# Performance work log

Measured on AMD Instinct MI355X. Metric: run time of the kernel, lower is better.

Reference implementation:

```python
import jax, jax.numpy as jnp
import numpy as np

B, S, E = 2, 2048, 2048
H, D = 16, 128  # num_heads, head_dim = E // H


def setup_inputs() -> dict:
    key = jax.random.key(0)
    ks = jax.random.split(key, 5)
    hidden_states = jax.random.normal(ks[0], (B, S, E), dtype=jnp.float32) * 0.02
    wq = jax.random.normal(ks[1], (E, E), dtype=jnp.float32) * 0.02
    wk = jax.random.normal(ks[2], (E, E), dtype=jnp.float32) * 0.02
    wv = jax.random.normal(ks[3], (E, E), dtype=jnp.float32) * 0.02
    wo = jax.random.normal(ks[4], (E, E), dtype=jnp.float32) * 0.02
    bo = jnp.zeros((E,), dtype=jnp.float32)
    return {"hidden_states": hidden_states, "wq": wq, "wk": wk, "wv": wv, "wo": wo, "bo": bo}


def _split_heads(x):
    # [B, S, E] -> [B, H, S, D]
    return x.reshape(B, S, H, D).transpose(0, 2, 1, 3)


def reference(hidden_states, wq, wk, wv, wo, bo):
    q = _split_heads(hidden_states @ wq)  # [B,H,S,D]
    k = _split_heads(hidden_states @ wk)
    v = _split_heads(hidden_states @ wv)

    # GPT-Neo: no 1/sqrt(d) scaling; scores computed in fp32
    attn_weights = jnp.einsum("bhqd,bhkd->bhqk", q.astype(jnp.float32), k.astype(jnp.float32))

    causal_mask = jnp.tril(jnp.ones((S, S), dtype=bool))  # bias[:, :, :S, :S]
    # Faithful quirk: masked positions get the GLOBAL MIN of attn_weights, not -inf
    mask_value = jnp.min(attn_weights)
    attn_weights = jnp.where(causal_mask, attn_weights, mask_value)

    attn_weights = jax.nn.softmax(attn_weights, axis=-1).astype(v.dtype)
    attn_output = jnp.einsum("bhqk,bhkd->bhqd", attn_weights, v)  # [B,H,S,D]

    # merge heads: [B,H,S,D] -> [B,S,E]
    attn_output = attn_output.transpose(0, 2, 1, 3).reshape(B, S, E)
    attn_output = attn_output @ wo + bo
    return attn_output
```

## Files before the change

kernel.cpp:

```cpp
#include <hip/hip_runtime.h>

typedef unsigned short u16;
typedef unsigned int   u32;
typedef __attribute__((ext_vector_type(4))) float f32x4;
typedef __attribute__((ext_vector_type(4))) u32   u32x4;
typedef __attribute__((ext_vector_type(8))) __bf16 bf16x8;

#define S_LEN 2048
#define EMB   2048
#define NH    16
#define HD    128
#define NBH   32
#define MTOT  4096

__device__ __forceinline__ u16 f2bf(float f) {
    u32 u = __float_as_uint(f);
    return (u16)((u + 0x7FFFu + ((u >> 16) & 1u)) >> 16);
}
__device__ __forceinline__ float bf2f(u16 v) {
    return __uint_as_float(((u32)v) << 16);
}
__device__ __forceinline__ bf16x8 ld_frag(const u16* p) {
    return __builtin_bit_cast(bf16x8, *(const u32x4*)p);
}
__device__ __forceinline__ void gld_lds16(const void* g, void* l) {
    __builtin_amdgcn_global_load_lds(
        (__attribute__((address_space(1))) void*)(g),
        (__attribute__((address_space(3))) void*)(l), 16, 0, 0);
}

__global__ __launch_bounds__(256) void cast_x_kernel(
    const float* __restrict__ X, u16* __restrict__ Xb)
{
    const size_t i = ((size_t)blockIdx.x * 256 + threadIdx.x) * 8;
    float4 a = *(const float4*)&X[i];
    float4 b = *(const float4*)&X[i + 4];
    u32x4 o;
    o.x = (u32)f2bf(a.x) | ((u32)f2bf(a.y) << 16);
    o.y = (u32)f2bf(a.z) | ((u32)f2bf(a.w) << 16);
    o.z = (u32)f2bf(b.x) | ((u32)f2bf(b.y) << 16);
    o.w = (u32)f2bf(b.z) | ((u32)f2bf(b.w) << 16);
    *(u32x4*)&Xb[i] = o;
}

__global__ __launch_bounds__(256) void transpose_cast_w_kernel(
    const float* __restrict__ W0, const float* __restrict__ W1,
    const float* __restrict__ W2, const float* __restrict__ W3,
    u16* __restrict__ T0, u16* __restrict__ T1,
    u16* __restrict__ T2, u16* __restrict__ T3)
{
    __shared__ float Ls[64][68];
    const int t = threadIdx.x;
    const int n0 = blockIdx.x * 64, k0 = blockIdx.y * 64;
    const int z = blockIdx.z;
    const float* __restrict__ W = (z == 0) ? W0 : (z == 1) ? W1 : (z == 2) ? W2 : W3;
    u16* __restrict__ T = (z == 0) ? T0 : (z == 1) ? T1 : (z == 2) ? T2 : T3;

#pragma unroll
    for (int p = 0; p < 4; ++p) {
        const int r = (t >> 4) + 16 * p;
        const int c = (t & 15) * 4;
        *(float4*)&Ls[r][c] = *(const float4*)&W[(size_t)(k0 + r) * EMB + n0 + c];
    }
    __syncthreads();
    const int nl = t >> 2, q = t & 3;
    u32 pk[8];
#pragma unroll
    for (int j = 0; j < 8; ++j) {
        u16 lo = f2bf(Ls[q * 16 + 2 * j][nl]);
        u16 hi = f2bf(Ls[q * 16 + 2 * j + 1][nl]);
        pk[j] = (u32)lo | ((u32)hi << 16);
    }
    u32x4 o0 = {pk[0], pk[1], pk[2], pk[3]};
    u32x4 o1 = {pk[4], pk[5], pk[6], pk[7]};
    u16* dst = &T[(size_t)(n0 + nl) * EMB + k0 + q * 16];
    *(u32x4*)&dst[0] = o0;
    *(u32x4*)&dst[8] = o1;
}

__global__ __launch_bounds__(256) void transpose_v_kernel(
    const u16* __restrict__ V, u16* __restrict__ Vt)
{
    __shared__ u16 Ls[64][72];
    const int t = threadIdx.x;
    const int s0 = blockIdx.x * 64, d0 = blockIdx.y * 64, bh = blockIdx.z;
    const u16* __restrict__ src0 = V + ((size_t)bh * S_LEN) * HD;
    {
        const int r = t >> 2, c0 = (t & 3) * 16;
        const u16* src = &src0[(size_t)(s0 + r) * HD + d0 + c0];
        *(u32x4*)&Ls[r][c0]     = *(const u32x4*)&src[0];
        *(u32x4*)&Ls[r][c0 + 8] = *(const u32x4*)&src[8];
    }
    __syncthreads();
    const int dl = t >> 2, q = t & 3;
    u32 pk[8];
#pragma unroll
    for (int j = 0; j < 8; ++j) {
        u16 lo = Ls[q * 16 + 2 * j][dl];
        u16 hi = Ls[q * 16 + 2 * j + 1][dl];
        pk[j] = (u32)lo | ((u32)hi << 16);
    }
    u32x4 o0 = {pk[0], pk[1], pk[2], pk[3]};
    u32x4 o1 = {pk[4], pk[5], pk[6], pk[7]};
    u16* dst = &Vt[((size_t)bh * HD + d0 + dl) * S_LEN + s0 + q * 16];
    *(u32x4*)&dst[0] = o0;
    *(u32x4*)&dst[8] = o1;
}

__global__ __launch_bounds__(256) void gemm_qkv_mfma(
    const u16* __restrict__ Xb,
    const u16* __restrict__ Wtq, const u16* __restrict__ Wtk,
    const u16* __restrict__ Wtv,
    u16* __restrict__ Qo, u16* __restrict__ Ko, u16* __restrict__ Vo)
{
    __shared__ __attribute__((aligned(16))) u16 As[128 * 32];
    __shared__ __attribute__((aligned(16))) u16 Bs[128 * 32];
    const int t = threadIdx.x;
    const int w = t >> 6, lane = t & 63;
    const int wy = w >> 1, wx = w & 1;
    const int n0 = blockIdx.x * 128, m0 = blockIdx.y * 128;
    const int z = blockIdx.z;
    const u16* __restrict__ Wt = (z == 0) ? Wtq : (z == 1) ? Wtk : Wtv;
    u16* __restrict__ O = (z == 0) ? Qo : (z == 1) ? Ko : Vo;

    const int srow = lane >> 2, scol = (lane & 3) * 8;
    const u16* Ag = &Xb[(size_t)(m0 + w * 32 + srow) * EMB + scol];
    const u16* Bg = &Wt[(size_t)(n0 + w * 32 + srow) * EMB + scol];
    u16* Al0 = &As[(w * 32) * 32];
    u16* Al1 = &As[(w * 32 + 16) * 32];
    u16* Bl0 = &Bs[(w * 32) * 32];
    u16* Bl1 = &Bs[(w * 32 + 16) * 32];

    const int fm = lane & 15, fk = (lane >> 4) * 8;
    f32x4 acc[4][4];
#pragma unroll
    for (int i = 0; i < 4; ++i)
#pragma unroll
        for (int j = 0; j < 4; ++j) acc[i][j] = (f32x4)0.0f;

    for (int k0 = 0; k0 < EMB; k0 += 32) {
        __syncthreads();
        gld_lds16(Ag + k0, Al0);
        gld_lds16(Ag + 16 * EMB + k0, Al1);
        gld_lds16(Bg + k0, Bl0);
        gld_lds16(Bg + 16 * EMB + k0, Bl1);
        __syncthreads();
        bf16x8 af[4], bfr[4];
#pragma unroll
        for (int mi = 0; mi < 4; ++mi)
            af[mi] = ld_frag(&As[(64 * wy + 16 * mi + fm) * 32 + fk]);
#pragma unroll
        for (int ni = 0; ni < 4; ++ni)
            bfr[ni] = ld_frag(&Bs[(64 * wx + 16 * ni + fm) * 32 + fk]);
#pragma unroll
        for (int mi = 0; mi < 4; ++mi)
#pragma unroll
            for (int ni = 0; ni < 4; ++ni)
                acc[mi][ni] = __builtin_amdgcn_mfma_f32_16x16x32_bf16(
                    af[mi], bfr[ni], acc[mi][ni], 0, 0, 0);
    }

    const int q4 = (lane >> 4) * 4;
#pragma unroll
    for (int mi = 0; mi < 4; ++mi)
#pragma unroll
        for (int ni = 0; ni < 4; ++ni) {
            const int n = n0 + 64 * wx + 16 * ni + (lane & 15);
            const int h = n >> 7, d = n & 127;
#pragma unroll
            for (int r = 0; r < 4; ++r) {
                const int m = m0 + 64 * wy + 16 * mi + q4 + r;
                const int bb = m >> 11, s = m & 2047;
                O[(((size_t)(bb * NH + h) * S_LEN) + s) * HD + d] = f2bf(acc[mi][ni][r]);
            }
        }
}

__global__ __launch_bounds__(256) void gemm_out_mfma(
    const u16* __restrict__ Ab, const u16* __restrict__ Wto,
    const float* __restrict__ bias, float* __restrict__ Out)
{
    __shared__ __attribute__((aligned(16))) u16 As[128 * 32];
    __shared__ __attribute__((aligned(16))) u16 Bs[128 * 32];
    const int t = threadIdx.x;
    const int w = t >> 6, lane = t & 63;
    const int wy = w >> 1, wx = w & 1;
    const int n0 = blockIdx.x * 128, m0 = blockIdx.y * 128;

    const int srow = lane >> 2, scol = (lane & 3) * 8;
    const u16* Ag = &Ab[(size_t)(m0 + w * 32 + srow) * EMB + scol];
    const u16* Bg = &Wto[(size_t)(n0 + w * 32 + srow) * EMB + scol];
    u16* Al0 = &As[(w * 32) * 32];
    u16* Al1 = &As[(w * 32 + 16) * 32];
    u16* Bl0 = &Bs[(w * 32) * 32];
    u16* Bl1 = &Bs[(w * 32 + 16) * 32];

    const int fm = lane & 15, fk = (lane >> 4) * 8;
    f32x4 acc[4][4];
#pragma unroll
    for (int i = 0; i < 4; ++i)
#pragma unroll
        for (int j = 0; j < 4; ++j) acc[i][j] = (f32x4)0.0f;

    for (int k0 = 0; k0 < EMB; k0 += 32) {
        __syncthreads();
        gld_lds16(Ag + k0, Al0);
        gld_lds16(Ag + 16 * EMB + k0, Al1);
        gld_lds16(Bg + k0, Bl0);
        gld_lds16(Bg + 16 * EMB + k0, Bl1);
        __syncthreads();
        bf16x8 af[4], bfr[4];
#pragma unroll
        for (int mi = 0; mi < 4; ++mi)
            af[mi] = ld_frag(&As[(64 * wy + 16 * mi + fm) * 32 + fk]);
#pragma unroll
        for (int ni = 0; ni < 4; ++ni)
            bfr[ni] = ld_frag(&Bs[(64 * wx + 16 * ni + fm) * 32 + fk]);
#pragma unroll
        for (int mi = 0; mi < 4; ++mi)
#pragma unroll
            for (int ni = 0; ni < 4; ++ni)
                acc[mi][ni] = __builtin_amdgcn_mfma_f32_16x16x32_bf16(
                    af[mi], bfr[ni], acc[mi][ni], 0, 0, 0);
    }

    const int q4 = (lane >> 4) * 4;
#pragma unroll
    for (int mi = 0; mi < 4; ++mi)
#pragma unroll
        for (int ni = 0; ni < 4; ++ni) {
            const int n = n0 + 64 * wx + 16 * ni + (lane & 15);
            const float bv = bias[n];
#pragma unroll
            for (int r = 0; r < 4; ++r) {
                const int m = m0 + 64 * wy + 16 * mi + q4 + r;
                Out[(size_t)m * EMB + n] = acc[mi][ni][r] + bv;
            }
        }
}

__global__ __launch_bounds__(256) void qk_min_mfma(
    const u16* __restrict__ Q, const u16* __restrict__ K,
    float* __restrict__ blockmin)
{
    __shared__ __attribute__((aligned(16))) u16 As[128 * 32];
    __shared__ __attribute__((aligned(16))) u16 Bs[128 * 32];
    __shared__ float sm[256];
    const int t = threadIdx.x;
    const int w = t >> 6, lane = t & 63;
    const int wy = w >> 1, wx = w & 1;
    const int kt = blockIdx.x, qt = blockIdx.y, bh = blockIdx.z;

    const int srow = lane >> 2, scol = (lane & 3) * 8;
    const u16* Ag = &Q[((size_t)bh * S_LEN + qt * 128 + w * 32 + srow) * HD + scol];
    const u16* Bg = &K[((size_t)bh * S_LEN + kt * 128 + w * 32 + srow) * HD + scol];
    u16* Al0 = &As[(w * 32) * 32];
    u16* Al1 = &As[(w * 32 + 16) * 32];
    u16* Bl0 = &Bs[(w * 32) * 32];
    u16* Bl1 = &Bs[(w * 32 + 16) * 32];

    const int fm = lane & 15, fk = (lane >> 4) * 8;
    f32x4 acc[4][4];
#pragma unroll
    for (int i = 0; i < 4; ++i)
#pragma unroll
        for (int j = 0; j < 4; ++j) acc[i][j] = (f32x4)0.0f;

    for (int k0 = 0; k0 < HD; k0 += 32) {
        __syncthreads();
        gld_lds16(Ag + k0, Al0);
        gld_lds16(Ag + 16 * HD + k0, Al1);
        gld_lds16(Bg + k0, Bl0);
        gld_lds16(Bg + 16 * HD + k0, Bl1);
        __syncthreads();
        bf16x8 af[4], bfr[4];
#pragma unroll
        for (int mi = 0; mi < 4; ++mi)
            af[mi] = ld_frag(&As[(64 * wy + 16 * mi + fm) * 32 + fk]);
#pragma unroll
        for (int ni = 0; ni < 4; ++ni)
            bfr[ni] = ld_frag(&Bs[(64 * wx + 16 * ni + fm) * 32 + fk]);
#pragma unroll
        for (int mi = 0; mi < 4; ++mi)
#pragma unroll
            for (int ni = 0; ni < 4; ++ni)
                acc[mi][ni] = __builtin_amdgcn_mfma_f32_16x16x32_bf16(
                    af[mi], bfr[ni], acc[mi][ni], 0, 0, 0);
    }

    float mn = acc[0][0][0];
#pragma unroll
    for (int mi = 0; mi < 4; ++mi)
#pragma unroll
        for (int ni = 0; ni < 4; ++ni)
#pragma unroll
            for (int r = 0; r < 4; ++r) mn = fminf(mn, acc[mi][ni][r]);
    sm[t] = mn;
    __syncthreads();
    for (int sft = 128; sft > 0; sft >>= 1) {
        if (t < sft) sm[t] = fminf(sm[t], sm[t + sft]);
        __syncthreads();
    }
    if (t == 0) blockmin[((size_t)bh * 16 + qt) * 16 + kt] = sm[0];
}

__global__ __launch_bounds__(256) void reduce_min_kernel(
    const float* __restrict__ bm, float* __restrict__ minval)
{
    __shared__ float sm[256];
    const int t = threadIdx.x;
    float m = 3.0e38f;
    for (int i = t; i < 16 * 16 * NBH; i += 256) m = fminf(m, bm[i]);
    sm[t] = m;
    __syncthreads();
    for (int sft = 128; sft > 0; sft >>= 1) {
        if (t < sft) sm[t] = fminf(sm[t], sm[t + sft]);
        __syncthreads();
    }
    if (t == 0) minval[0] = sm[0];
}

__global__ __launch_bounds__(128) void vchunk_sum_kernel(
    const u16* __restrict__ V, float* __restrict__ csum)
{
    const int chunk = blockIdx.x, bh = blockIdx.y, d = threadIdx.x;
    const u16* vb = V + ((size_t)bh * S_LEN + chunk * 64) * HD + d;
    float s = 0.0f;
    for (int r = 0; r < 64; ++r) s += bf2f(vb[(size_t)r * HD]);
    csum[((size_t)bh * 32 + chunk) * HD + d] = s;
}

__global__ __launch_bounds__(128) void vchunk_suffix_kernel(
    const float* __restrict__ csum, float* __restrict__ csuf)
{
    const int bh = blockIdx.x, d = threadIdx.x;
    float run = 0.0f;
    for (int c = 31; c >= 0; --c) {
        const size_t idx = ((size_t)bh * 32 + c) * HD + d;
        csuf[idx] = run;
        run += csum[idx];
    }
}

__global__ __launch_bounds__(128) void vsuffix_kernel(
    const u16* __restrict__ V, const float* __restrict__ csuf,
    float* __restrict__ vsuf)
{
    const int chunk = blockIdx.x, bh = blockIdx.y, d = threadIdx.x;
    float run = csuf[((size_t)bh * 32 + chunk) * HD + d];
    const size_t base = ((size_t)bh * S_LEN + chunk * 64) * HD + d;
    for (int r = 63; r >= 0; --r) {
        vsuf[base + (size_t)r * HD] = run;
        run += bf2f(V[base + (size_t)r * HD]);
    }
}

__global__ __launch_bounds__(256) void attn_mfma(
    const u16* __restrict__ Q, const u16* __restrict__ K,
    const u16* __restrict__ Vt, const float* __restrict__ vsuf,
    const float* __restrict__ minval, u16* __restrict__ outm)
{
    __shared__ __attribute__((aligned(16))) u16 Qs[128 * 136];
    __shared__ __attribute__((aligned(16))) u16 Ps[128 * 136];
    __shared__ __attribute__((aligned(16))) u16 Cs[128 * 32];
    __shared__ float den_l[2][128];

    const int t = threadIdx.x;
    const int w = t >> 6, lane = t & 63;
    const int wy = w >> 1, wx = w & 1;
    const int qt = blockIdx.x, bh = blockIdx.y;
    const int b = bh >> 4, h = bh & 15;
    const int i0 = qt * 128;

    const u16* __restrict__ Qg  = Q + ((size_t)bh * S_LEN + i0) * HD;
    const u16* __restrict__ Kg  = K + (size_t)bh * S_LEN * HD;
    const u16* __restrict__ Vtg = Vt + (size_t)bh * HD * S_LEN;

    {
        const int r = t >> 1, ch = (t & 1) * 64;
        const u16* src = &Qg[(size_t)r * HD + ch];
        u16* dst = &Qs[r * 136 + ch];
#pragma unroll
        for (int j = 0; j < 8; ++j)
            *(u32x4*)&dst[j * 8] = *(const u32x4*)&src[j * 8];
    }

    const int srow = lane >> 2, scol = (lane & 3) * 8;
    const int fm = lane & 15, fk = (lane >> 4) * 8;
    const int q4 = (lane >> 4) * 4;

    f32x4 oacc[4][4];
#pragma unroll
    for (int i = 0; i < 4; ++i)
#pragma unroll
        for (int j = 0; j < 4; ++j) oacc[i][j] = (f32x4)0.0f;
    float den[4][4] = {};

    const int ntile = qt + 1;
    for (int jt = 0; jt < ntile; ++jt) {
        const int j0 = jt * 128;
        f32x4 sacc[4][4];
#pragma unroll
        for (int i = 0; i < 4; ++i)
#pragma unroll
            for (int j = 0; j < 4; ++j) sacc[i][j] = (f32x4)0.0f;
        for (int dk = 0; dk < 4; ++dk) {
            __syncthreads();
            {
                const u16* g = &Kg[(size_t)(j0 + w * 32 + srow) * HD + dk * 32 + scol];
                gld_lds16(g, &Cs[(w * 32) * 32]);
                gld_lds16(g + 16 * HD, &Cs[(w * 32 + 16) * 32]);
            }
            __syncthreads();
            bf16x8 af[4], bfr[4];
#pragma unroll
            for (int mi = 0; mi < 4; ++mi)
                af[mi] = ld_frag(&Qs[(64 * wy + 16 * mi + fm) * 136 + dk * 32 + fk]);
#pragma unroll
            for (int ni = 0; ni < 4; ++ni)
                bfr[ni] = ld_frag(&Cs[(64 * wx + 16 * ni + fm) * 32 + fk]);
#pragma unroll
            for (int mi = 0; mi < 4; ++mi)
#pragma unroll
                for (int ni = 0; ni < 4; ++ni)
                    sacc[mi][ni] = __builtin_amdgcn_mfma_f32_16x16x32_bf16(
                        af[mi], bfr[ni], sacc[mi][ni], 0, 0, 0);
        }
        const bool dg = (jt == qt);
#pragma unroll
        for (int mi = 0; mi < 4; ++mi) {
            const int rbase = 64 * wy + 16 * mi + q4;
#pragma unroll
            for (int ni = 0; ni < 4; ++ni) {
                const int cl = 64 * wx + 16 * ni + (lane & 15);
                const int jg = j0 + cl;
#pragma unroll
                for (int r = 0; r < 4; ++r) {
                    float e = __expf(sacc[mi][ni][r]);
                    if (dg && jg > i0 + rbase + r) e = 0.0f;
                    den[mi][r] += e;
                    Ps[(rbase + r) * 136 + cl] = f2bf(e);
                }
            }
        }
        for (int sk = 0; sk < 4; ++sk) {
            __syncthreads();
            {
                const u16* g = &Vtg[(size_t)(w * 32 + srow) * S_LEN + j0 + sk * 32 + scol];
                gld_lds16(g, &Cs[(w * 32) * 32]);
                gld_lds16(g + 16 * S_LEN, &Cs[(w * 32 + 16) * 32]);
            }
            __syncthreads();
            bf16x8 pa[4], pb[4];
#pragma unroll
            for (int mi = 0; mi < 4; ++mi)
                pa[mi] = ld_frag(&Ps[(64 * wy + 16 * mi + fm) * 136 + sk * 32 + fk]);
#pragma unroll
            for (int ni = 0; ni < 4; ++ni)
                pb[ni] = ld_frag(&Cs[(64 * wx + 16 * ni + fm) * 32 + fk]);
#pragma unroll
            for (int mi = 0; mi < 4; ++mi)
#pragma unroll
                for (int ni = 0; ni < 4; ++ni)
                    oacc[mi][ni] = __builtin_amdgcn_mfma_f32_16x16x32_bf16(
                        pa[mi], pb[ni], oacc[mi][ni], 0, 0, 0);
        }
    }

#pragma unroll
    for (int mi = 0; mi < 4; ++mi)
#pragma unroll
        for (int r = 0; r < 4; ++r) {
            float v = den[mi][r];
            v += __shfl_xor(v, 1, 64);
            v += __shfl_xor(v, 2, 64);
            v += __shfl_xor(v, 4, 64);
            v += __shfl_xor(v, 8, 64);
            den[mi][r] = v;
        }
    __syncthreads();
    if ((lane & 15) == 0) {
#pragma unroll
        for (int mi = 0; mi < 4; ++mi)
#pragma unroll
            for (int r = 0; r < 4; ++r)
                den_l[wx][64 * wy + 16 * mi + q4 + r] = den[mi][r];
    }
    __syncthreads();

    const float em = __expf(minval[0]);
#pragma unroll
    for (int mi = 0; mi < 4; ++mi)
#pragma unroll
        for (int ni = 0; ni < 4; ++ni) {
            const int d = 64 * wx + 16 * ni + (lane & 15);
#pragma unroll
            for (int r = 0; r < 4; ++r) {
                const int row = 64 * wy + 16 * mi + q4 + r;
                const int ig = i0 + row;
                const float dt = den_l[0][row] + den_l[1][row]
                               + (float)(S_LEN - 1 - ig) * em;
                const float sv = vsuf[((size_t)bh * S_LEN + ig) * HD + d];
                const float o = (oacc[mi][ni][r] + em * sv) / dt;
                outm[((size_t)b * S_LEN + ig) * EMB + h * HD + d] = f2bf(o);
            }
        }
}

extern "C" void kernel_launch(void* const* d_in, const int* in_sizes, int n_in,
                              void* d_out, int out_size, void* d_ws, size_t ws_size,
                              hipStream_t stream)
{
    (void)in_sizes; (void)n_in; (void)out_size; (void)ws_size;
    const float* hs = (const float*)d_in[0];
    const float* wq = (const float*)d_in[1];
    const float* wk = (const float*)d_in[2];
    const float* wv = (const float*)d_in[3];
    const float* wo = (const float*)d_in[4];
    const float* bo = (const float*)d_in[5];
    float* out = (float*)d_out;

    char* p = (char*)d_ws;
    const size_t TS = (size_t)NBH * S_LEN * HD;
    u16* Xb   = (u16*)p; p += (size_t)MTOT * EMB * 2;
    u16* Wtq  = (u16*)p; p += (size_t)EMB * EMB * 2;
    u16* Wtk  = (u16*)p; p += (size_t)EMB * EMB * 2;
    u16* Wtv  = (u16*)p; p += (size_t)EMB * EMB * 2;
    u16* Wto  = (u16*)p; p += (size_t)EMB * EMB * 2;
    u16* Qb   = (u16*)p; p += TS * 2;
    u16* Kb   = (u16*)p; p += TS * 2;
    u16* Vb   = (u16*)p; p += TS * 2;
    u16* Vtb  = (u16*)p; p += TS * 2;
    u16* outm = (u16*)p; p += (size_t)MTOT * EMB * 2;
    float* vsuf     = (float*)p; p += TS * 4;
    float* csum     = (float*)p; p += (size_t)NBH * 32 * HD * 4;
    float* csuf     = (float*)p; p += (size_t)NBH * 32 * HD * 4;
    float* blockmin = (float*)p; p += 8192 * 4;
    float* minval   = (float*)p; p += 64;

    cast_x_kernel<<<4096, 256, 0, stream>>>(hs, Xb);
    transpose_cast_w_kernel<<<dim3(32, 32, 4), 256, 0, stream>>>(
        wq, wk, wv, wo, Wtq, Wtk, Wtv, Wto);

    gemm_qkv_mfma<<<dim3(EMB / 128, MTOT / 128, 3), 256, 0, stream>>>(
        Xb, Wtq, Wtk, Wtv, Qb, Kb, Vb);

    transpose_v_kernel<<<dim3(32, 2, NBH), 256, 0, stream>>>(Vb, Vtb);
    vchunk_sum_kernel<<<dim3(32, NBH), 128, 0, stream>>>(Vb, csum);
    vchunk_suffix_kernel<<<NBH, 128, 0, stream>>>(csum, csuf);
    vsuffix_kernel<<<dim3(32, NBH), 128, 0, stream>>>(Vb, csuf, vsuf);

    qk_min_mfma<<<dim3(16, 16, NBH), 256, 0, stream>>>(Qb, Kb, blockmin);
    reduce_min_kernel<<<1, 256, 0, stream>>>(blockmin, minval);

    attn_mfma<<<dim3(S_LEN / 128, NBH), 256, 0, stream>>>(
        Qb, Kb, Vtb, vsuf, minval, outm);

    gemm_out_mfma<<<dim3(EMB / 128, MTOT / 128), 256, 0, stream>>>(
        outm, Wto, bo, out);
}
```

Baseline: 482.6 us.

## Fuse lower-triangle min into attention and balance causal tiles with split-K passes

The global-min pass now only computes QK scores for strictly upper-triangular tiles. The attention kernel computes the lower-triangle minimum as it goes, which removes the duplicated score work. The attention grid pairs query tile pp with tile 15-pp to balance causal work across blocks. Each pair is split by key-tile parity into two partial accumulators, stored in bf16 together with partial denominators. A new finalize kernel then combines the partials with the suffix-V correction and the global min. This adds extra memory traffic and an extra bf16 rounding of the partial outputs.

```diff
diff --git a/kernel.cpp b/kernel.cpp
--- a/kernel.cpp
+++ b/kernel.cpp
@@ -12,6 +12,8 @@
 #define HD    128
 #define NBH   32
 #define MTOT  4096
+#define NUP   120
+#define NBMIN (NBH * NUP + 512)
 
 __device__ __forceinline__ u16 f2bf(float f) {
     u32 u = __float_as_uint(f);
@@ -239,7 +241,7 @@
         }
 }
 
-__global__ __launch_bounds__(256) void qk_min_mfma(
+__global__ __launch_bounds__(256) void qk_upper_min(
     const u16* __restrict__ Q, const u16* __restrict__ K,
     float* __restrict__ blockmin)
 {
@@ -249,7 +251,10 @@
     const int t = threadIdx.x;
     const int w = t >> 6, lane = t & 63;
     const int wy = w >> 1, wx = w & 1;
-    const int kt = blockIdx.x, qt = blockIdx.y, bh = blockIdx.z;
+    int u = blockIdx.x, qt = 0, cnt = 15;
+    while (u >= cnt) { u -= cnt; ++qt; cnt = 15 - qt; }
+    const int kt = qt + 1 + u;
+    const int bh = blockIdx.y;
 
     const int srow = lane >> 2, scol = (lane & 3) * 8;
     const u16* Ag = &Q[((size_t)bh * S_LEN + qt * 128 + w * 32 + srow) * HD + scol];
@@ -301,7 +306,7 @@
         if (t < sft) sm[t] = fminf(sm[t], sm[t + sft]);
         __syncthreads();
     }
-    if (t == 0) blockmin[((size_t)bh * 16 + qt) * 16 + kt] = sm[0];
+    if (t == 0) blockmin[(size_t)bh * NUP + blockIdx.x] = sm[0];
 }
 
 __global__ __launch_bounds__(256) void reduce_min_kernel(
@@ -310,7 +315,7 @@
     __shared__ float sm[256];
     const int t = threadIdx.x;
     float m = 3.0e38f;
-    for (int i = t; i < 16 * 16 * NBH; i += 256) m = fminf(m, bm[i]);
+    for (int i = t; i < NBMIN; i += 256) m = fminf(m, bm[i]);
     sm[t] = m;
     __syncthreads();
     for (int sft = 128; sft > 0; sft >>= 1) {
@@ -357,154 +362,205 @@
 
 __global__ __launch_bounds__(256) void attn_mfma(
     const u16* __restrict__ Q, const u16* __restrict__ K,
-    const u16* __restrict__ Vt, const float* __restrict__ vsuf,
-    const float* __restrict__ minval, u16* __restrict__ outm)
+    const u16* __restrict__ Vt,
+    u16* __restrict__ pacc0, u16* __restrict__ pacc1,
+    float* __restrict__ den_p, float* __restrict__ blockmin)
 {
     __shared__ __attribute__((aligned(16))) u16 Qs[128 * 136];
     __shared__ __attribute__((aligned(16))) u16 Ps[128 * 136];
     __shared__ __attribute__((aligned(16))) u16 Cs[128 * 32];
     __shared__ float den_l[2][128];
+    __shared__ float smn[256];
 
     const int t = threadIdx.x;
     const int w = t >> 6, lane = t & 63;
     const int wy = w >> 1, wx = w & 1;
-    const int qt = blockIdx.x, bh = blockIdx.y;
+    const int pp = blockIdx.x >> 1, hpar = blockIdx.x & 1;
+    const int bh = blockIdx.y;
     const int b = bh >> 4, h = bh & 15;
-    const int i0 = qt * 128;
-
-    const u16* __restrict__ Qg  = Q + ((size_t)bh * S_LEN + i0) * HD;
+
     const u16* __restrict__ Kg  = K + (size_t)bh * S_LEN * HD;
     const u16* __restrict__ Vtg = Vt + (size_t)bh * HD * S_LEN;
-
-    {
-        const int r = t >> 1, ch = (t & 1) * 64;
-        const u16* src = &Qg[(size_t)r * HD + ch];
-        u16* dst = &Qs[r * 136 + ch];
-#pragma unroll
-        for (int j = 0; j < 8; ++j)
-            *(u32x4*)&dst[j * 8] = *(const u32x4*)&src[j * 8];
-    }
+    u16* __restrict__ pacc = hpar ? pacc1 : pacc0;
 
     const int srow = lane >> 2, scol = (lane & 3) * 8;
     const int fm = lane & 15, fk = (lane >> 4) * 8;
     const int q4 = (lane >> 4) * 4;
 
-    f32x4 oacc[4][4];
-#pragma unroll
-    for (int i = 0; i < 4; ++i)
-#pragma unroll
-        for (int j = 0; j < 4; ++j) oacc[i][j] = (f32x4)0.0f;
-    float den[4][4] = {};
-
-    const int ntile = qt + 1;
-    for (int jt = 0; jt < ntile; ++jt) {
-        const int j0 = jt * 128;
-        f32x4 sacc[4][4];
+    float mn = 3.0e38f;
+
+    for (int pass = 0; pass < 2; ++pass) {
+        const int qt = pass ? (15 - pp) : pp;
+        const int i0 = qt * 128;
+        const u16* __restrict__ Qg = Q + ((size_t)bh * S_LEN + i0) * HD;
+
+        __syncthreads();
+        {
+            const int r = t >> 1, ch = (t & 1) * 64;
+            const u16* src = &Qg[(size_t)r * HD + ch];
+            u16* dst = &Qs[r * 136 + ch];
+#pragma unroll
+            for (int j = 0; j < 8; ++j)
+                *(u32x4*)&dst[j * 8] = *(const u32x4*)&src[j * 8];
+        }
+
+        f32x4 oacc[4][4];
 #pragma unroll
         for (int i = 0; i < 4; ++i)
 #pragma unroll
-            for (int j = 0; j < 4; ++j) sacc[i][j] = (f32x4)0.0f;
-        for (int dk = 0; dk < 4; ++dk) {
-            __syncthreads();
-            {
-                const u16* g = &Kg[(size_t)(j0 + w * 32 + srow) * HD + dk * 32 + scol];
-                gld_lds16(g, &Cs[(w * 32) * 32]);
-                gld_lds16(g + 16 * HD, &Cs[(w * 32 + 16) * 32]);
+            for (int j = 0; j < 4; ++j) oacc[i][j] = (f32x4)0.0f;
+        float den[4][4] = {};
+
+        for (int jt = hpar; jt <= qt; jt += 2) {
+            const int j0 = jt * 128;
+            f32x4 sacc[4][4];
+#pragma unroll
+            for (int i = 0; i < 4; ++i)
+#pragma unroll
+                for (int j = 0; j < 4; ++j) sacc[i][j] = (f32x4)0.0f;
+            for (int dk = 0; dk < 4; ++dk) {
+                __syncthreads();
+                {
+                    const u16* g = &Kg[(size_t)(j0 + w * 32 + srow) * HD + dk * 32 + scol];
+                    gld_lds16(g, &Cs[(w * 32) * 32]);
+                    gld_lds16(g + 16 * HD, &Cs[(w * 32 + 16) * 32]);
+                }
+                __syncthreads();
+                bf16x8 af[4], bfr[4];
+#pragma unroll
+                for (int mi = 0; mi < 4; ++mi)
+                    af[mi] = ld_frag(&Qs[(64 * wy + 16 * mi + fm) * 136 + dk * 32 + fk]);
+#pragma unroll
+                for (int ni = 0; ni < 4; ++ni)
+                    bfr[ni] = ld_frag(&Cs[(64 * wx + 16 * ni + fm) * 32 + fk]);
+#pragma unroll
+                for (int mi = 0; mi < 4; ++mi)
+#pragma unroll
+                    for (int ni = 0; ni < 4; ++ni)
+                        sacc[mi][ni] = __builtin_amdgcn_mfma_f32_16x16x32_bf16(
+                            af[mi], bfr[ni], sacc[mi][ni], 0, 0, 0);
+            }
+            const bool dg = (jt == qt);
+#pragma unroll
+            for (int mi = 0; mi < 4; ++mi) {
+                const int rbase = 64 * wy + 16 * mi + q4;
+#pragma unroll
+                for (int ni = 0; ni < 4; ++ni) {
+                    const int cl = 64 * wx + 16 * ni + (lane & 15);
+                    const int jg = j0 + cl;
+#pragma unroll
+                    for (int r = 0; r < 4; ++r) {
+                        const float s = sacc[mi][ni][r];
+                        mn = fminf(mn, s);
+                        float e = __expf(s);
+                        if (dg && jg > i0 + rbase + r) e = 0.0f;
+                        den[mi][r] += e;
+                        Ps[(rbase + r) * 136 + cl] = f2bf(e);
+                    }
+                }
             }
             __syncthreads();
-            bf16x8 af[4], bfr[4];
+
+            for (int sk = 0; sk < 4; ++sk) {
+                if (sk) __syncthreads();
+                {
+                    const u16* g = &Vtg[(size_t)(w * 32 + srow) * S_LEN + j0 + sk * 32 + scol];
+                    gld_lds16(g, &Cs[(w * 32) * 32]);
+                    gld_lds16(g + 16 * S_LEN, &Cs[(w * 32 + 16) * 32]);
+                }
+                __syncthreads();
+                bf16x8 pa[4], pb[4];
+#pragma unroll
+                for (int mi = 0; mi < 4; ++mi)
+                    pa[mi] = ld_frag(&Ps[(64 * wy + 16 * mi + fm) * 136 + sk * 32 + fk]);
+#pragma unroll
+                for (int ni = 0; ni < 4; ++ni)
+                    pb[ni] = ld_frag(&Cs[(64 * wx + 16 * ni + fm) * 32 + fk]);
+#pragma unroll
+                for (int mi = 0; mi < 4; ++mi)
+#pragma unroll
+                    for (int ni = 0; ni < 4; ++ni)
+                        oacc[mi][ni] = __builtin_amdgcn_mfma_f32_16x16x32_bf16(
+                            pa[mi], pb[ni], oacc[mi][ni], 0, 0, 0);
+            }
+        }
+
+#pragma unroll
+        for (int mi = 0; mi < 4; ++mi)
+#pragma unroll
+            for (int r = 0; r < 4; ++r) {
+                float v = den[mi][r];
+                v += __shfl_xor(v, 1, 64);
+                v += __shfl_xor(v, 2, 64);
+                v += __shfl_xor(v, 4, 64);
+                v += __shfl_xor(v, 8, 64);
+                den[mi][r] = v;
+            }
+        __syncthreads();
+        if ((lane & 15) == 0) {
 #pragma unroll
             for (int mi = 0; mi < 4; ++mi)
-                af[mi] = ld_frag(&Qs[(64 * wy + 16 * mi + fm) * 136 + dk * 32 + fk]);
-#pragma unroll
-            for (int ni = 0; ni < 4; ++ni)
-                bfr[ni] = ld_frag(&Cs[(64 * wx + 16 * ni + fm) * 32 + fk]);
-#pragma unroll
-            for (int mi = 0; mi < 4; ++mi)
-#pragma unroll
-                for (int ni = 0; ni < 4; ++ni)
-                    sacc[mi][ni] = __builtin_amdgcn_mfma_f32_16x16x32_bf16(
-                        af[mi], bfr[ni], sacc[mi][ni], 0, 0, 0);
+#pragma unroll
+                for (int r = 0; r < 4; ++r)
+                    den_l[wx][64 * wy + 16 * mi + q4 + r] = den[mi][r];
         }
-        const bool dg = (jt == qt);
-#pragma unroll
-        for (int mi = 0; mi < 4; ++mi) {
-            const int rbase = 64 * wy + 16 * mi + q4;
+        __syncthreads();
+        if (t < 128)
+            den_p[((size_t)hpar * NBH + bh) * S_LEN + i0 + t] =
+                den_l[0][t] + den_l[1][t];
+
+#pragma unroll
+        for (int mi = 0; mi < 4; ++mi)
 #pragma unroll
             for (int ni = 0; ni < 4; ++ni) {
-                const int cl = 64 * wx + 16 * ni + (lane & 15);
-                const int jg = j0 + cl;
+                const int d = 64 * wx + 16 * ni + (lane & 15);
 #pragma unroll
                 for (int r = 0; r < 4; ++r) {
-                    float e = __expf(sacc[mi][ni][r]);
-                    if (dg && jg > i0 + rbase + r) e = 0.0f;
-                    den[mi][r] += e;
-                    Ps[(rbase + r) * 136 + cl] = f2bf(e);
+                    const int row = 64 * wy + 16 * mi + q4 + r;
+                    pacc[((size_t)b * S_LEN + i0 + row) * EMB + h * HD + d] =
+                        f2bf(oacc[mi][ni][r]);
                 }
             }
-        }
-        for (int sk = 0; sk < 4; ++sk) {
-            __syncthreads();
-            {
-                const u16* g = &Vtg[(size_t)(w * 32 + srow) * S_LEN + j0 + sk * 32 + scol];
-                gld_lds16(g, &Cs[(w * 32) * 32]);
-                gld_lds16(g + 16 * S_LEN, &Cs[(w * 32 + 16) * 32]);
-            }
-            __syncthreads();
-            bf16x8 pa[4], pb[4];
-#pragma unroll
-            for (int mi = 0; mi < 4; ++mi)
-                pa[mi] = ld_frag(&Ps[(64 * wy + 16 * mi + fm) * 136 + sk * 32 + fk]);
-#pragma unroll
-            for (int ni = 0; ni < 4; ++ni)
-                pb[ni] = ld_frag(&Cs[(64 * wx + 16 * ni + fm) * 32 + fk]);
-#pragma unroll
-            for (int mi = 0; mi < 4; ++mi)
-#pragma unroll
-                for (int ni = 0; ni < 4; ++ni)
-                    oacc[mi][ni] = __builtin_amdgcn_mfma_f32_16x16x32_bf16(
-                        pa[mi], pb[ni], oacc[mi][ni], 0, 0, 0);
-        }
-    }
-
-#pragma unroll
-    for (int mi = 0; mi < 4; ++mi)
-#pragma unroll
-        for (int r = 0; r < 4; ++r) {
-            float v = den[mi][r];
-            v += __shfl_xor(v, 1, 64);
-            v += __shfl_xor(v, 2, 64);
-            v += __shfl_xor(v, 4, 64);
-            v += __shfl_xor(v, 8, 64);
-            den[mi][r] = v;
-        }
+    }
+
     __syncthreads();
-    if ((lane & 15) == 0) {
-#pragma unroll
-        for (int mi = 0; mi < 4; ++mi)
-#pragma unroll
-            for (int r = 0; r < 4; ++r)
-                den_l[wx][64 * wy + 16 * mi + q4 + r] = den[mi][r];
-    }
+    smn[t] = mn;
     __syncthreads();
-
+    for (int sft = 128; sft > 0; sft >>= 1) {
+        if (t < sft) smn[t] = fminf(smn[t], smn[t + sft]);
+        __syncthreads();
+    }
+    if (t == 0) blockmin[blockIdx.y * 16 + blockIdx.x] = smn[0];
+}
+
+__global__ __launch_bounds__(256) void finalize_kernel(
+    u16* __restrict__ outm, const u16* __restrict__ pacc1,
+    const float* __restrict__ vsuf, const float* __restrict__ den_p,
+    const float* __restrict__ minval)
+{
+    const size_t i = ((size_t)blockIdx.x * 256 + threadIdx.x) * 8;
+    const int e = (int)(i & (EMB - 1));
+    const int m = (int)(i / EMB);
+    const int b = m >> 11, s = m & 2047;
+    const int hh = e >> 7, d = e & 127;
+    const int bh = b * NH + hh;
     const float em = __expf(minval[0]);
-#pragma unroll
-    for (int mi = 0; mi < 4; ++mi)
-#pragma unroll
-        for (int ni = 0; ni < 4; ++ni) {
-            const int d = 64 * wx + 16 * ni + (lane & 15);
-#pragma unroll
-            for (int r = 0; r < 4; ++r) {
-                const int row = 64 * wy + 16 * mi + q4 + r;
-                const int ig = i0 + row;
-                const float dt = den_l[0][row] + den_l[1][row]
-                               + (float)(S_LEN - 1 - ig) * em;
-                const float sv = vsuf[((size_t)bh * S_LEN + ig) * HD + d];
-                const float o = (oacc[mi][ni][r] + em * sv) / dt;
-                outm[((size_t)b * S_LEN + ig) * EMB + h * HD + d] = f2bf(o);
-            }
-        }
+    const float den = den_p[(size_t)bh * S_LEN + s]
+                    + den_p[((size_t)NBH + bh) * S_LEN + s]
+                    + (float)(S_LEN - 1 - s) * em;
+    const float inv = 1.0f / den;
+    u32x4 a = *(const u32x4*)&outm[i];
+    u32x4 c = *(const u32x4*)&pacc1[i];
+    const u16* pa = (const u16*)&a;
+    const u16* pc = (const u16*)&c;
+    const float* vs = &vsuf[((size_t)bh * S_LEN + s) * HD + d];
+    u16 ov[8];
+#pragma unroll
+    for (int j = 0; j < 8; ++j) {
+        const float v = bf2f(pa[j]) + bf2f(pc[j]) + em * vs[j];
+        ov[j] = f2bf(v * inv);
+    }
+    *(u32x4*)&outm[i] = *(const u32x4*)ov;
 }
 
 extern "C" void kernel_launch(void* const* d_in, const int* in_sizes, int n_in,
@@ -537,6 +593,8 @@
     float* csuf     = (float*)p; p += (size_t)NBH * 32 * HD * 4;
     float* blockmin = (float*)p; p += 8192 * 4;
     float* minval   = (float*)p; p += 64;
+    float* den_p    = (float*)p; p += (size_t)2 * NBH * S_LEN * 4;
+    u16* pacc1 = Xb;
 
     cast_x_kernel<<<4096, 256, 0, stream>>>(hs, Xb);
     transpose_cast_w_kernel<<<dim3(32, 32, 4), 256, 0, stream>>>(
@@ -550,11 +608,15 @@
     vchunk_suffix_kernel<<<NBH, 128, 0, stream>>>(csum, csuf);
     vsuffix_kernel<<<dim3(32, NBH), 128, 0, stream>>>(Vb, csuf, vsuf);
 
-    qk_min_mfma<<<dim3(16, 16, NBH), 256, 0, stream>>>(Qb, Kb, blockmin);
+    qk_upper_min<<<dim3(NUP, NBH), 256, 0, stream>>>(Qb, Kb, blockmin);
+
+    attn_mfma<<<dim3(16, NBH), 256, 0, stream>>>(
+        Qb, Kb, Vtb, outm, pacc1, den_p, blockmin + (size_t)NBH * NUP);
+
     reduce_min_kernel<<<1, 256, 0, stream>>>(blockmin, minval);
 
-    attn_mfma<<<dim3(S_LEN / 128, NBH), 256, 0, stream>>>(
-        Qb, Kb, Vtb, vsuf, minval, outm);
+    finalize_kernel<<<(MTOT * EMB / 8) / 256, 256, 0, stream>>>(
+        outm, pacc1, vsuf, den_p, minval);
 
     gemm_out_mfma<<<dim3(EMB / 128, MTOT / 128), 256, 0, stream>>>(
         outm, Wto, bo, out);
```

Result: slower. 494.6 us (+2.5%).
